# Kernel optimization log

Measured on AMD Instinct MI355X. Metric: run time of the kernel, lower is better.

The kernel has to match this reference:

```python
import jax, jax.numpy as jnp
import numpy as np

EPS_RMS = 1e-6
Q_CLIP_MIN = 1e-5

def setup_inputs() -> dict:
    key = jax.random.key(0)
    k1, k2 = jax.random.split(key)
    x = jax.random.normal(k1, (1, 2048, 4096), dtype=jnp.float32)
    # kaiming_uniform-ish init for weight [in_features, out_features]
    fan_in = 4096
    bound = 1.0 / np.sqrt(fan_in)
    weight = jax.random.uniform(k2, (4096, 4096), dtype=jnp.float32, minval=-bound, maxval=bound)
    rms_weight = jnp.ones((4096,), dtype=jnp.float32)
    return {"x": x, "weight": weight, "rms_weight": rms_weight}

def reference(x, weight, rms_weight):
    # RMSNorm over last dim
    xn = x * jax.lax.rsqrt(jnp.mean(x * x, axis=-1, keepdims=True) + EPS_RMS) * rms_weight
    K = weight.shape[0]
    orig_shape = xn.shape
    x2 = xn.reshape(-1, K)  # [M, K]

    # per-tensor absmax int8 activation quantization
    a_scale = 127.0 / jnp.clip(jnp.max(jnp.abs(x2)), Q_CLIP_MIN)
    A_q = jnp.clip(jnp.round(x2 * a_scale), -128.0, 127.0)

    # absmean ternary weight quantization
    b_scale = 1.0 / jnp.clip(jnp.mean(jnp.abs(weight)), Q_CLIP_MIN)
    B_t = jnp.clip(jnp.round(weight * b_scale), -1.0, 1.0)

    # integer matmul + dequant: (A_q @ B_t) / (a_scale * b_scale)
    out = (A_q @ B_t) / (a_scale * b_scale)  # [M, N]
    return out.reshape(*orig_shape[:-1], weight.shape[1])
```

## Files before the change

kernel.cpp:

```cpp
#include <hip/hip_runtime.h>
#include <cstdint>

#define M_DIM 2048
#define K_DIM 4096
#define N_DIM 4096

#define BM 256
#define BN 128
#define BK 128
#define KT (K_DIM / BK)
#define A_TILE_BYTES (BM * BK)
#define B_TILE_BYTES (BN * BK)
#define TILE_BYTES (A_TILE_BYTES + B_TILE_BYTES)
#define NBUF 3
#define LDS_BYTES (NBUF * TILE_BYTES)

typedef __attribute__((ext_vector_type(4))) int i32x4;

__device__ __forceinline__ void gload_lds16(const void* g, void* l) {
  __builtin_amdgcn_global_load_lds(
      (__attribute__((address_space(1))) void*)(g),
      (__attribute__((address_space(3))) void*)(l), 16, 0, 0);
}

__global__ void fused_reduce_kernel(const float* __restrict__ x,
                                    const float* __restrict__ rw,
                                    const float* __restrict__ w,
                                    float* __restrict__ invrms,
                                    float* __restrict__ rowmax,
                                    double* __restrict__ partials) {
  const int tid = threadIdx.x;
  __shared__ double red[4];
  __shared__ float redf[4];
  __shared__ float sInv;

  if (blockIdx.x < 2048) {
    const int row = blockIdx.x;
    const float4* xr = (const float4*)(x + (size_t)row * K_DIM);
    const float4* wr = (const float4*)rw;
    float4 xv[4];
    double ss = 0.0;
#pragma unroll
    for (int i = 0; i < 4; i++) {
      xv[i] = xr[i * 256 + tid];
      ss += (double)xv[i].x * xv[i].x + (double)xv[i].y * xv[i].y +
            (double)xv[i].z * xv[i].z + (double)xv[i].w * xv[i].w;
    }
    for (int off = 32; off; off >>= 1) ss += __shfl_down(ss, off);
    if ((tid & 63) == 0) red[tid >> 6] = ss;
    __syncthreads();
    if (tid == 0) {
      double t = red[0] + red[1] + red[2] + red[3];
      sInv = (float)(1.0 / sqrt(t * (1.0 / (double)K_DIM) + 1e-6));
    }
    __syncthreads();
    const float inv = sInv;
    if (tid == 0) invrms[row] = inv;

    float amax = 0.f;
#pragma unroll
    for (int i = 0; i < 4; i++) {
      float4 wv = wr[i * 256 + tid];
      amax = fmaxf(amax, fabsf((xv[i].x * inv) * wv.x));
      amax = fmaxf(amax, fabsf((xv[i].y * inv) * wv.y));
      amax = fmaxf(amax, fabsf((xv[i].z * inv) * wv.z));
      amax = fmaxf(amax, fabsf((xv[i].w * inv) * wv.w));
    }
    for (int off = 32; off; off >>= 1) amax = fmaxf(amax, __shfl_down(amax, off));
    if ((tid & 63) == 0) redf[tid >> 6] = amax;
    __syncthreads();
    if (tid == 0)
      rowmax[row] = fmaxf(fmaxf(redf[0], redf[1]), fmaxf(redf[2], redf[3]));
  } else {
    const int bid = blockIdx.x - 2048;
    const float4* w4 = (const float4*)w;
    const size_t base = (size_t)bid * 2048;
    double s = 0.0;
#pragma unroll
    for (int i = 0; i < 8; i++) {
      float4 v = w4[base + i * 256 + tid];
      s += (double)((fabsf(v.x) + fabsf(v.y)) + (fabsf(v.z) + fabsf(v.w)));
    }
    for (int off = 32; off; off >>= 1) s += __shfl_down(s, off);
    if ((tid & 63) == 0) red[tid >> 6] = s;
    __syncthreads();
    if (tid == 0) partials[bid] = red[0] + red[1] + red[2] + red[3];
  }
}

__global__ void scales_kernel(const float* __restrict__ rowmax,
                              const double* __restrict__ partials,
                              float* __restrict__ scales) {
  const int tid = threadIdx.x;
  float m = 0.f;
  double s = 0.0;
#pragma unroll
  for (int i = 0; i < 8; i++) {
    m = fmaxf(m, rowmax[i * 256 + tid]);
    s += partials[i * 256 + tid];
  }
  for (int off = 32; off; off >>= 1) {
    m = fmaxf(m, __shfl_down(m, off));
    s += __shfl_down(s, off);
  }
  __shared__ float redf[4];
  __shared__ double red[4];
  if ((tid & 63) == 0) { redf[tid >> 6] = m; red[tid >> 6] = s; }
  __syncthreads();
  if (tid == 0) {
    float amax = fmaxf(fmaxf(redf[0], redf[1]), fmaxf(redf[2], redf[3]));
    double wsum = red[0] + red[1] + red[2] + red[3];
    float as = 127.0f / fmaxf(amax, 1e-5f);
    float mean_f = (float)(wsum * (1.0 / 16777216.0));
    float bs = 1.0f / fmaxf(mean_f, 1e-5f);
    scales[0] = as;
    scales[1] = bs;
    scales[2] = 1.0f / (as * bs);
  }
}

__global__ void fused_quant_kernel(const float* __restrict__ x,
                                   const float* __restrict__ rw,
                                   const float* __restrict__ invrms,
                                   const float* __restrict__ scales,
                                   const float* __restrict__ w,
                                   char* __restrict__ Aq,
                                   char* __restrict__ Bt) {
  const int tid = threadIdx.x;
  if (blockIdx.x < 2048) {
    const int row = blockIdx.x;
    const float inv = invrms[row];
    const float as = scales[0];
    const float4* xr = (const float4*)(x + (size_t)row * K_DIM);
    const float4* wr = (const float4*)rw;
    union { char c[16]; int4 v; } o;
#pragma unroll
    for (int i = 0; i < 4; i++) {
      float4 xv = xr[tid * 4 + i];
      float4 wv = wr[tid * 4 + i];
      float t0 = (xv.x * inv) * wv.x;
      float t1 = (xv.y * inv) * wv.y;
      float t2 = (xv.z * inv) * wv.z;
      float t3 = (xv.w * inv) * wv.w;
      o.c[i * 4 + 0] = (char)(int)fminf(fmaxf(rintf(t0 * as), -128.f), 127.f);
      o.c[i * 4 + 1] = (char)(int)fminf(fmaxf(rintf(t1 * as), -128.f), 127.f);
      o.c[i * 4 + 2] = (char)(int)fminf(fmaxf(rintf(t2 * as), -128.f), 127.f);
      o.c[i * 4 + 3] = (char)(int)fminf(fmaxf(rintf(t3 * as), -128.f), 127.f);
    }
    *(int4*)(Aq + (size_t)row * K_DIM + tid * 16) = o.v;
  } else {
    __shared__ float lds[64][68];
    const int tile = blockIdx.x - 2048;
    const int n0 = (tile & 63) * 64;
    const int k0 = (tile >> 6) * 64;
    const float bs = scales[1];
#pragma unroll
    for (int i = 0; i < 4; i++) {
      const int id = i * 256 + tid;
      const int r = id >> 4;
      const int c4 = (id & 15) * 4;
      float4 v = *(const float4*)(w + (size_t)(k0 + r) * N_DIM + n0 + c4);
      lds[c4 + 0][r] = fminf(fmaxf(rintf(v.x * bs), -1.f), 1.f);
      lds[c4 + 1][r] = fminf(fmaxf(rintf(v.y * bs), -1.f), 1.f);
      lds[c4 + 2][r] = fminf(fmaxf(rintf(v.z * bs), -1.f), 1.f);
      lds[c4 + 3][r] = fminf(fmaxf(rintf(v.w * bs), -1.f), 1.f);
    }
    __syncthreads();
    const int rn = tid >> 2;
    const int kg = (tid & 3) * 16;
    union { char c[16]; int4 v; } o;
#pragma unroll
    for (int j = 0; j < 16; j++) o.c[j] = (char)(int)lds[rn][kg + j];
    *(int4*)(Bt + (size_t)(n0 + rn) * K_DIM + k0 + kg) = o.v;
  }
}

__global__ void __launch_bounds__(512, 2)
gemm_kernel(const char* __restrict__ Aq, const char* __restrict__ Bt,
            float* __restrict__ out, const float* __restrict__ scales) {
  extern __shared__ char lds[];
  const int tid = threadIdx.x;
  const int lane = tid & 63;
  const int wave = tid >> 6;
  const int wm = wave >> 1;
  const int wn = wave & 1;
  const int brow = blockIdx.y * BM;
  const int bcol = blockIdx.x * BN;

  i32x4 acc[4][4];
#pragma unroll
  for (int m = 0; m < 4; m++)
#pragma unroll
    for (int n = 0; n < 4; n++) acc[m][n] = {0, 0, 0, 0};

  const int sRow8 = lane >> 3;
  const int srcColB = ((lane & 7) ^ sRow8) * 16;

#define STAGE_A(kt, bi, s)                                                        \
  gload_lds16(Aq + (size_t)(brow + (s)*64 + wave * 8 + sRow8) * K_DIM +           \
                  (kt)*BK + srcColB,                                              \
              lds + (bi)*TILE_BYTES + (s)*8192 + wave * 1024 + lane * 16)
#define STAGE_B(kt, bi, s)                                                        \
  gload_lds16(Bt + (size_t)(bcol + (s)*64 + wave * 8 + sRow8) * K_DIM +           \
                  (kt)*BK + srcColB,                                              \
              lds + (bi)*TILE_BYTES + A_TILE_BYTES + (s)*8192 + wave * 1024 +     \
                  lane * 16)

  STAGE_A(0, 0, 0); STAGE_A(0, 0, 1); STAGE_A(0, 0, 2); STAGE_A(0, 0, 3);
  STAGE_B(0, 0, 0); STAGE_B(0, 0, 1);
  STAGE_A(1, 1, 0); STAGE_A(1, 1, 1); STAGE_A(1, 1, 2); STAGE_A(1, 1, 3);
  STAGE_B(1, 1, 0); STAGE_B(1, 1, 1);

  const int frow = lane & 15;
  int bi = 0;
  for (int t = 0; t < KT; ++t) {
    if (t < KT - 1) {
      asm volatile("s_waitcnt vmcnt(6)" ::: "memory");
    } else {
      asm volatile("s_waitcnt vmcnt(0)" ::: "memory");
    }
    __builtin_amdgcn_s_barrier();

    const int si = (bi + 2 >= NBUF) ? bi + 2 - NBUF : bi + 2;
    const bool doStage = (t + 2) < KT;
    const char* bufA = lds + bi * TILE_BYTES;
    const char* bufB = bufA + A_TILE_BYTES;

    if (doStage) {
      STAGE_A(t + 2, si, 0); STAGE_A(t + 2, si, 1); STAGE_A(t + 2, si, 2);
    }
    {
      const int sc = ((0 * 4 + (lane >> 4)) ^ (lane & 7)) * 16;
      i32x4 a[4], b[4];
#pragma unroll
      for (int m = 0; m < 4; m++)
        a[m] = *(const i32x4*)(bufA + (wm * 64 + m * 16 + frow) * BK + sc);
#pragma unroll
      for (int n = 0; n < 4; n++)
        b[n] = *(const i32x4*)(bufB + (wn * 64 + n * 16 + frow) * BK + sc);
      __builtin_amdgcn_s_setprio(1);
#pragma unroll
      for (int m = 0; m < 4; m++)
#pragma unroll
        for (int n = 0; n < 4; n++)
          acc[m][n] = __builtin_amdgcn_mfma_i32_16x16x64_i8(a[m], b[n], acc[m][n], 0, 0, 0);
      __builtin_amdgcn_s_setprio(0);
    }
    if (doStage) {
      STAGE_A(t + 2, si, 3); STAGE_B(t + 2, si, 0); STAGE_B(t + 2, si, 1);
    }
    {
      const int sc = ((1 * 4 + (lane >> 4)) ^ (lane & 7)) * 16;
      i32x4 a[4], b[4];
#pragma unroll
      for (int m = 0; m < 4; m++)
        a[m] = *(const i32x4*)(bufA + (wm * 64 + m * 16 + frow) * BK + sc);
#pragma unroll
      for (int n = 0; n < 4; n++)
        b[n] = *(const i32x4*)(bufB + (wn * 64 + n * 16 + frow) * BK + sc);
      __builtin_amdgcn_s_setprio(1);
#pragma unroll
      for (int m = 0; m < 4; m++)
#pragma unroll
        for (int n = 0; n < 4; n++)
          acc[m][n] = __builtin_amdgcn_mfma_i32_16x16x64_i8(a[m], b[n], acc[m][n], 0, 0, 0);
      __builtin_amdgcn_s_setprio(0);
    }
    bi = (bi + 1 >= NBUF) ? 0 : bi + 1;
  }
#undef STAGE_A
#undef STAGE_B

  const float dq = scales[2];
#pragma unroll
  for (int m = 0; m < 4; m++) {
#pragma unroll
    for (int n = 0; n < 4; n++) {
      const int row = wm * 64 + m * 16 + (lane >> 4) * 4;
      const int col = wn * 64 + n * 16 + (lane & 15);
#pragma unroll
      for (int j = 0; j < 4; j++) {
        out[(size_t)(brow + row + j) * N_DIM + bcol + col] = (float)acc[m][n][j] * dq;
      }
    }
  }
}

extern "C" void kernel_launch(void* const* d_in, const int* in_sizes, int n_in,
                              void* d_out, int out_size, void* d_ws, size_t ws_size,
                              hipStream_t stream) {
  const float* x      = (const float*)d_in[0];
  const float* weight = (const float*)d_in[1];
  const float* rms_w  = (const float*)d_in[2];
  float* out = (float*)d_out;

  uint8_t* ws = (uint8_t*)d_ws;
  float* scales   = (float*)(ws + 0);
  float* invrms   = (float*)(ws + 64);
  float* rowmax   = (float*)(ws + 64 + 8192);
  double* partials = (double*)(ws + 64 + 16384);
  char* Aq = (char*)(ws + 65536);
  char* Bt = (char*)(ws + 65536 + (size_t)M_DIM * K_DIM);

  (void)hipFuncSetAttribute((const void*)gemm_kernel,
                            hipFuncAttributeMaxDynamicSharedMemorySize, LDS_BYTES);

  fused_reduce_kernel<<<4096, 256, 0, stream>>>(x, rms_w, weight, invrms, rowmax, partials);
  scales_kernel<<<1, 256, 0, stream>>>(rowmax, partials, scales);
  fused_quant_kernel<<<6144, 256, 0, stream>>>(x, rms_w, invrms, scales, weight, Aq, Bt);
  gemm_kernel<<<dim3(N_DIM / BN, M_DIM / BM), 512, LDS_BYTES, stream>>>(Aq, Bt, out, scales);
}
```

Measured before the change: 74.34 us.

## Restructure GEMM K-loop into four-quadrant ping-pong schedule with interleaved staging

Reorganizes the int8 GEMM main loop so each wave loads A/B fragments for both K sub-steps per 64x64 quadrant, then runs MFMAs over four 32x32 quadrants while interleaving global-to-LDS staging between them. The intent is to overlap LDS reads and async global loads with MFMA execution, using explicit barriers, lgkmcnt waits and sched_barriers to pin the instruction order. It adds several workgroup barriers per iteration and holds more fragment registers at once, which could hurt occupancy or add sync stalls. The wait and barrier for the first tile is moved ahead of the loop, and the vmcnt wait now sits at the end of each iteration.

New measurement: 77.32 us. +4.0%, slower.

```diff
diff --git a/kernel.cpp b/kernel.cpp
--- a/kernel.cpp
+++ b/kernel.cpp
@@ -210,10 +210,98 @@
   STAGE_B(0, 0, 0); STAGE_B(0, 0, 1);
   STAGE_A(1, 1, 0); STAGE_A(1, 1, 1); STAGE_A(1, 1, 2); STAGE_A(1, 1, 3);
   STAGE_B(1, 1, 0); STAGE_B(1, 1, 1);
-
-  const int frow = lane & 15;
+  asm volatile("s_waitcnt vmcnt(6)" ::: "memory");
+  __builtin_amdgcn_s_barrier();
+
+  const int aBase = (wm * 64 + (lane & 15)) * BK;
+  const int bBase = (wn * 64 + (lane & 15)) * BK;
+  const int swz0 = ((0 * 4 + (lane >> 4)) ^ (lane & 7)) * 16;
+  const int swz1 = ((1 * 4 + (lane >> 4)) ^ (lane & 7)) * 16;
+
   int bi = 0;
   for (int t = 0; t < KT; ++t) {
+    const char* bufA = lds + bi * TILE_BYTES;
+    const char* bufB = bufA + A_TILE_BYTES;
+    const int si = (bi + 2 >= NBUF) ? bi + 2 - NBUF : bi + 2;
+    const bool doStage = (t + 2) < KT;
+
+    i32x4 a0_[4], a1_[4], b0_[4], b1_[4];
+
+#pragma unroll
+    for (int s = 0; s < 2; s++) {
+      a0_[s * 2 + 0] = *(const i32x4*)(bufA + aBase + s * 2048 + swz0);
+      a0_[s * 2 + 1] = *(const i32x4*)(bufA + aBase + s * 2048 + swz1);
+      b0_[s * 2 + 0] = *(const i32x4*)(bufB + bBase + s * 2048 + swz0);
+      b0_[s * 2 + 1] = *(const i32x4*)(bufB + bBase + s * 2048 + swz1);
+    }
+    if (doStage) { STAGE_A(t + 2, si, 0); STAGE_A(t + 2, si, 1); }
+    __builtin_amdgcn_s_barrier();
+    asm volatile("s_waitcnt lgkmcnt(0)" ::: "memory");
+    __builtin_amdgcn_sched_barrier(0);
+    __builtin_amdgcn_s_setprio(1);
+#pragma unroll
+    for (int mi = 0; mi < 2; mi++)
+#pragma unroll
+      for (int ni = 0; ni < 2; ni++)
+#pragma unroll
+        for (int ks = 0; ks < 2; ks++)
+          acc[mi][ni] = __builtin_amdgcn_mfma_i32_16x16x64_i8(
+              a0_[mi * 2 + ks], b0_[ni * 2 + ks], acc[mi][ni], 0, 0, 0);
+    __builtin_amdgcn_s_setprio(0);
+    __builtin_amdgcn_s_barrier();
+
+#pragma unroll
+    for (int s = 0; s < 2; s++) {
+      b1_[s * 2 + 0] = *(const i32x4*)(bufB + bBase + (s + 2) * 2048 + swz0);
+      b1_[s * 2 + 1] = *(const i32x4*)(bufB + bBase + (s + 2) * 2048 + swz1);
+    }
+    if (doStage) { STAGE_A(t + 2, si, 2); STAGE_A(t + 2, si, 3); }
+    __builtin_amdgcn_s_barrier();
+    asm volatile("s_waitcnt lgkmcnt(0)" ::: "memory");
+    __builtin_amdgcn_sched_barrier(0);
+    __builtin_amdgcn_s_setprio(1);
+#pragma unroll
+    for (int mi = 0; mi < 2; mi++)
+#pragma unroll
+      for (int ni = 0; ni < 2; ni++)
+#pragma unroll
+        for (int ks = 0; ks < 2; ks++)
+          acc[mi][ni + 2] = __builtin_amdgcn_mfma_i32_16x16x64_i8(
+              a0_[mi * 2 + ks], b1_[ni * 2 + ks], acc[mi][ni + 2], 0, 0, 0);
+    __builtin_amdgcn_s_setprio(0);
+    __builtin_amdgcn_s_barrier();
+
+#pragma unroll
+    for (int s = 0; s < 2; s++) {
+      a1_[s * 2 + 0] = *(const i32x4*)(bufA + aBase + (s + 2) * 2048 + swz0);
+      a1_[s * 2 + 1] = *(const i32x4*)(bufA + aBase + (s + 2) * 2048 + swz1);
+    }
+    if (doStage) { STAGE_B(t + 2, si, 0); STAGE_B(t + 2, si, 1); }
+    __builtin_amdgcn_s_barrier();
+    asm volatile("s_waitcnt lgkmcnt(0)" ::: "memory");
+    __builtin_amdgcn_sched_barrier(0);
+    __builtin_amdgcn_s_setprio(1);
+#pragma unroll
+    for (int mi = 0; mi < 2; mi++)
+#pragma unroll
+      for (int ni = 0; ni < 2; ni++)
+#pragma unroll
+        for (int ks = 0; ks < 2; ks++)
+          acc[mi + 2][ni] = __builtin_amdgcn_mfma_i32_16x16x64_i8(
+              a1_[mi * 2 + ks], b0_[ni * 2 + ks], acc[mi + 2][ni], 0, 0, 0);
+    __builtin_amdgcn_s_setprio(0);
+    __builtin_amdgcn_s_barrier();
+
+    __builtin_amdgcn_s_setprio(1);
+#pragma unroll
+    for (int mi = 0; mi < 2; mi++)
+#pragma unroll
+      for (int ni = 0; ni < 2; ni++)
+#pragma unroll
+        for (int ks = 0; ks < 2; ks++)
+          acc[mi + 2][ni + 2] = __builtin_amdgcn_mfma_i32_16x16x64_i8(
+              a1_[mi * 2 + ks], b1_[ni * 2 + ks], acc[mi + 2][ni + 2], 0, 0, 0);
+    __builtin_amdgcn_s_setprio(0);
     if (t < KT - 1) {
       asm volatile("s_waitcnt vmcnt(6)" ::: "memory");
     } else {
@@ -221,51 +309,6 @@
     }
     __builtin_amdgcn_s_barrier();
 
-    const int si = (bi + 2 >= NBUF) ? bi + 2 - NBUF : bi + 2;
-    const bool doStage = (t + 2) < KT;
-    const char* bufA = lds + bi * TILE_BYTES;
-    const char* bufB = bufA + A_TILE_BYTES;
-
-    if (doStage) {
-      STAGE_A(t + 2, si, 0); STAGE_A(t + 2, si, 1); STAGE_A(t + 2, si, 2);
-    }
-    {
-      const int sc = ((0 * 4 + (lane >> 4)) ^ (lane & 7)) * 16;
-      i32x4 a[4], b[4];
-#pragma unroll
-      for (int m = 0; m < 4; m++)
-        a[m] = *(const i32x4*)(bufA + (wm * 64 + m * 16 + frow) * BK + sc);
-#pragma unroll
-      for (int n = 0; n < 4; n++)
-        b[n] = *(const i32x4*)(bufB + (wn * 64 + n * 16 + frow) * BK + sc);
-      __builtin_amdgcn_s_setprio(1);
-#pragma unroll
-      for (int m = 0; m < 4; m++)
-#pragma unroll
-        for (int n = 0; n < 4; n++)
-          acc[m][n] = __builtin_amdgcn_mfma_i32_16x16x64_i8(a[m], b[n], acc[m][n], 0, 0, 0);
-      __builtin_amdgcn_s_setprio(0);
-    }
-    if (doStage) {
-      STAGE_A(t + 2, si, 3); STAGE_B(t + 2, si, 0); STAGE_B(t + 2, si, 1);
-    }
-    {
-      const int sc = ((1 * 4 + (lane >> 4)) ^ (lane & 7)) * 16;
-      i32x4 a[4], b[4];
-#pragma unroll
-      for (int m = 0; m < 4; m++)
-        a[m] = *(const i32x4*)(bufA + (wm * 64 + m * 16 + frow) * BK + sc);
-#pragma unroll
-      for (int n = 0; n < 4; n++)
-        b[n] = *(const i32x4*)(bufB + (wn * 64 + n * 16 + frow) * BK + sc);
-      __builtin_amdgcn_s_setprio(1);
-#pragma unroll
-      for (int m = 0; m < 4; m++)
-#pragma unroll
-        for (int n = 0; n < 4; n++)
-          acc[m][n] = __builtin_amdgcn_mfma_i32_16x16x64_i8(a[m], b[n], acc[m][n], 0, 0, 0);
-      __builtin_amdgcn_s_setprio(0);
-    }
     bi = (bi + 1 >= NBUF) ? 0 : bi + 1;
   }
 #undef STAGE_A
@@ -295,9 +338,9 @@
   float* out = (float*)d_out;
 
   uint8_t* ws = (uint8_t*)d_ws;
-  float* scales   = (float*)(ws + 0);
-  float* invrms   = (float*)(ws + 64);
-  float* rowmax   = (float*)(ws + 64 + 8192);
+  float* scales    = (float*)(ws + 0);
+  float* invrms    = (float*)(ws + 64);
+  float* rowmax    = (float*)(ws + 64 + 8192);
   double* partials = (double*)(ws + 64 + 16384);
   char* Aq = (char*)(ws + 65536);
   char* Bt = (char*)(ws + 65536 + (size_t)M_DIM * K_DIM);
```

## Use four-wave GEMM blocks with 128x64 warp tiles and fragment prefetch

Applied to the files above, without the earlier changes.

Restructures the int8 GEMM from 8 waves computing 64x64 each to 4 waves computing 128x64 each, and processes the full BK=128 slice per iteration with two k-substeps. The goal is to raise MFMA-to-LDS-read reuse per wave. The A/B fragments for the next tile are loaded into registers before the next iteration, and explicit lgkmcnt/vmcnt waits with sched_barriers overlap LDS reads with MFMA work. The cost is a much larger register footprint and fewer waves per CU to hide latency.

Result: slower. 77.04 us (+3.6%).

```diff
diff --git a/kernel.cpp b/kernel.cpp
--- a/kernel.cpp
+++ b/kernel.cpp
@@ -175,7 +175,7 @@
   }
 }
 
-__global__ void __launch_bounds__(512, 2)
+__global__ void __launch_bounds__(256, 1)
 gemm_kernel(const char* __restrict__ Aq, const char* __restrict__ Bt,
             float* __restrict__ out, const float* __restrict__ scales) {
   extern __shared__ char lds[];
@@ -187,9 +187,9 @@
   const int brow = blockIdx.y * BM;
   const int bcol = blockIdx.x * BN;
 
-  i32x4 acc[4][4];
-#pragma unroll
-  for (int m = 0; m < 4; m++)
+  i32x4 acc[8][4];
+#pragma unroll
+  for (int m = 0; m < 8; m++)
 #pragma unroll
     for (int n = 0; n < 4; n++) acc[m][n] = {0, 0, 0, 0};
 
@@ -197,74 +197,113 @@
   const int srcColB = ((lane & 7) ^ sRow8) * 16;
 
 #define STAGE_A(kt, bi, s)                                                        \
-  gload_lds16(Aq + (size_t)(brow + (s)*64 + wave * 8 + sRow8) * K_DIM +           \
+  gload_lds16(Aq + (size_t)(brow + (s)*32 + wave * 8 + sRow8) * K_DIM +           \
                   (kt)*BK + srcColB,                                              \
-              lds + (bi)*TILE_BYTES + (s)*8192 + wave * 1024 + lane * 16)
+              lds + (bi)*TILE_BYTES + (s)*4096 + wave * 1024 + lane * 16)
 #define STAGE_B(kt, bi, s)                                                        \
-  gload_lds16(Bt + (size_t)(bcol + (s)*64 + wave * 8 + sRow8) * K_DIM +           \
+  gload_lds16(Bt + (size_t)(bcol + (s)*32 + wave * 8 + sRow8) * K_DIM +           \
                   (kt)*BK + srcColB,                                              \
-              lds + (bi)*TILE_BYTES + A_TILE_BYTES + (s)*8192 + wave * 1024 +     \
+              lds + (bi)*TILE_BYTES + A_TILE_BYTES + (s)*4096 + wave * 1024 +     \
                   lane * 16)
 
-  STAGE_A(0, 0, 0); STAGE_A(0, 0, 1); STAGE_A(0, 0, 2); STAGE_A(0, 0, 3);
-  STAGE_B(0, 0, 0); STAGE_B(0, 0, 1);
-  STAGE_A(1, 1, 0); STAGE_A(1, 1, 1); STAGE_A(1, 1, 2); STAGE_A(1, 1, 3);
-  STAGE_B(1, 1, 0); STAGE_B(1, 1, 1);
-
-  const int frow = lane & 15;
+#pragma unroll
+  for (int s = 0; s < 8; s++) STAGE_A(0, 0, s);
+#pragma unroll
+  for (int s = 0; s < 4; s++) STAGE_B(0, 0, s);
+#pragma unroll
+  for (int s = 0; s < 8; s++) STAGE_A(1, 1, s);
+#pragma unroll
+  for (int s = 0; s < 4; s++) STAGE_B(1, 1, s);
+  asm volatile("s_waitcnt vmcnt(12)" ::: "memory");
+  __builtin_amdgcn_s_barrier();
+
+  const int aBase = (wm * 128 + (lane & 15)) * BK;
+  const int bBase = (wn * 64 + (lane & 15)) * BK;
+  const int swz0 = ((0 + (lane >> 4)) ^ (lane & 7)) * 16;
+  const int swz1 = ((4 + (lane >> 4)) ^ (lane & 7)) * 16;
+
+  i32x4 a0[8], a1[8], bb[8];
+
+#pragma unroll
+  for (int m = 0; m < 4; m++) {
+    a0[m * 2 + 0] = *(const i32x4*)(lds + aBase + m * 2048 + swz0);
+    a0[m * 2 + 1] = *(const i32x4*)(lds + aBase + m * 2048 + swz1);
+  }
+#pragma unroll
+  for (int n = 0; n < 4; n++) {
+    bb[n * 2 + 0] = *(const i32x4*)(lds + A_TILE_BYTES + bBase + n * 2048 + swz0);
+    bb[n * 2 + 1] = *(const i32x4*)(lds + A_TILE_BYTES + bBase + n * 2048 + swz1);
+  }
+
   int bi = 0;
   for (int t = 0; t < KT; ++t) {
-    if (t < KT - 1) {
-      asm volatile("s_waitcnt vmcnt(6)" ::: "memory");
-    } else {
-      asm volatile("s_waitcnt vmcnt(0)" ::: "memory");
-    }
-    __builtin_amdgcn_s_barrier();
-
+    const char* bufA = lds + bi * TILE_BYTES;
     const int si = (bi + 2 >= NBUF) ? bi + 2 - NBUF : bi + 2;
     const bool doStage = (t + 2) < KT;
-    const char* bufA = lds + bi * TILE_BYTES;
-    const char* bufB = bufA + A_TILE_BYTES;
+
+    __builtin_amdgcn_s_barrier();
+    __builtin_amdgcn_sched_barrier(0);
 
     if (doStage) {
       STAGE_A(t + 2, si, 0); STAGE_A(t + 2, si, 1); STAGE_A(t + 2, si, 2);
-    }
-    {
-      const int sc = ((0 * 4 + (lane >> 4)) ^ (lane & 7)) * 16;
-      i32x4 a[4], b[4];
-#pragma unroll
-      for (int m = 0; m < 4; m++)
-        a[m] = *(const i32x4*)(bufA + (wm * 64 + m * 16 + frow) * BK + sc);
+      STAGE_A(t + 2, si, 3); STAGE_A(t + 2, si, 4); STAGE_A(t + 2, si, 5);
+    }
+#pragma unroll
+    for (int m = 0; m < 4; m++) {
+      a1[m * 2 + 0] = *(const i32x4*)(bufA + aBase + (m + 4) * 2048 + swz0);
+      a1[m * 2 + 1] = *(const i32x4*)(bufA + aBase + (m + 4) * 2048 + swz1);
+    }
+    asm volatile("s_waitcnt lgkmcnt(8)" ::: "memory");
+    __builtin_amdgcn_sched_barrier(0);
+    __builtin_amdgcn_s_setprio(1);
+#pragma unroll
+    for (int m = 0; m < 4; m++)
 #pragma unroll
       for (int n = 0; n < 4; n++)
-        b[n] = *(const i32x4*)(bufB + (wn * 64 + n * 16 + frow) * BK + sc);
-      __builtin_amdgcn_s_setprio(1);
-#pragma unroll
-      for (int m = 0; m < 4; m++)
-#pragma unroll
-        for (int n = 0; n < 4; n++)
-          acc[m][n] = __builtin_amdgcn_mfma_i32_16x16x64_i8(a[m], b[n], acc[m][n], 0, 0, 0);
-      __builtin_amdgcn_s_setprio(0);
-    }
+#pragma unroll
+        for (int ks = 0; ks < 2; ks++)
+          acc[m][n] = __builtin_amdgcn_mfma_i32_16x16x64_i8(
+              a0[m * 2 + ks], bb[n * 2 + ks], acc[m][n], 0, 0, 0);
+    __builtin_amdgcn_s_setprio(0);
+
     if (doStage) {
-      STAGE_A(t + 2, si, 3); STAGE_B(t + 2, si, 0); STAGE_B(t + 2, si, 1);
-    }
-    {
-      const int sc = ((1 * 4 + (lane >> 4)) ^ (lane & 7)) * 16;
-      i32x4 a[4], b[4];
-#pragma unroll
-      for (int m = 0; m < 4; m++)
-        a[m] = *(const i32x4*)(bufA + (wm * 64 + m * 16 + frow) * BK + sc);
+      STAGE_A(t + 2, si, 6); STAGE_A(t + 2, si, 7);
+      STAGE_B(t + 2, si, 0); STAGE_B(t + 2, si, 1);
+      STAGE_B(t + 2, si, 2); STAGE_B(t + 2, si, 3);
+    }
+    asm volatile("s_waitcnt lgkmcnt(0)" ::: "memory");
+    __builtin_amdgcn_sched_barrier(0);
+    __builtin_amdgcn_s_setprio(1);
+#pragma unroll
+    for (int m = 0; m < 4; m++)
 #pragma unroll
       for (int n = 0; n < 4; n++)
-        b[n] = *(const i32x4*)(bufB + (wn * 64 + n * 16 + frow) * BK + sc);
-      __builtin_amdgcn_s_setprio(1);
-#pragma unroll
-      for (int m = 0; m < 4; m++)
-#pragma unroll
-        for (int n = 0; n < 4; n++)
-          acc[m][n] = __builtin_amdgcn_mfma_i32_16x16x64_i8(a[m], b[n], acc[m][n], 0, 0, 0);
-      __builtin_amdgcn_s_setprio(0);
+#pragma unroll
+        for (int ks = 0; ks < 2; ks++)
+          acc[m + 4][n] = __builtin_amdgcn_mfma_i32_16x16x64_i8(
+              a1[m * 2 + ks], bb[n * 2 + ks], acc[m + 4][n], 0, 0, 0);
+    __builtin_amdgcn_s_setprio(0);
+
+    if (t + 1 < KT) {
+      if (doStage) {
+        asm volatile("s_waitcnt vmcnt(12)" ::: "memory");
+      } else {
+        asm volatile("s_waitcnt vmcnt(0)" ::: "memory");
+      }
+      __builtin_amdgcn_sched_barrier(0);
+      const int ni = (bi + 1 >= NBUF) ? 0 : bi + 1;
+      const char* nA = lds + ni * TILE_BYTES;
+      const char* nB = nA + A_TILE_BYTES;
+#pragma unroll
+      for (int m = 0; m < 4; m++) {
+        a0[m * 2 + 0] = *(const i32x4*)(nA + aBase + m * 2048 + swz0);
+        a0[m * 2 + 1] = *(const i32x4*)(nA + aBase + m * 2048 + swz1);
+      }
+#pragma unroll
+      for (int n = 0; n < 4; n++) {
+        bb[n * 2 + 0] = *(const i32x4*)(nB + bBase + n * 2048 + swz0);
+        bb[n * 2 + 1] = *(const i32x4*)(nB + bBase + n * 2048 + swz1);
+      }
     }
     bi = (bi + 1 >= NBUF) ? 0 : bi + 1;
   }
@@ -273,10 +312,10 @@
 
   const float dq = scales[2];
 #pragma unroll
-  for (int m = 0; m < 4; m++) {
+  for (int m = 0; m < 8; m++) {
 #pragma unroll
     for (int n = 0; n < 4; n++) {
-      const int row = wm * 64 + m * 16 + (lane >> 4) * 4;
+      const int row = wm * 128 + m * 16 + (lane >> 4) * 4;
       const int col = wn * 64 + n * 16 + (lane & 15);
 #pragma unroll
       for (int j = 0; j < 4; j++) {
@@ -295,9 +334,9 @@
   float* out = (float*)d_out;
 
   uint8_t* ws = (uint8_t*)d_ws;
-  float* scales   = (float*)(ws + 0);
-  float* invrms   = (float*)(ws + 64);
-  float* rowmax   = (float*)(ws + 64 + 8192);
+  float* scales    = (float*)(ws + 0);
+  float* invrms    = (float*)(ws + 64);
+  float* rowmax    = (float*)(ws + 64 + 8192);
   double* partials = (double*)(ws + 64 + 16384);
   char* Aq = (char*)(ws + 65536);
   char* Bt = (char*)(ws + 65536 + (size_t)M_DIM * K_DIM);
@@ -308,5 +347,5 @@
   fused_reduce_kernel<<<4096, 256, 0, stream>>>(x, rms_w, weight, invrms, rowmax, partials);
   scales_kernel<<<1, 256, 0, stream>>>(rowmax, partials, scales);
   fused_quant_kernel<<<6144, 256, 0, stream>>>(x, rms_w, invrms, scales, weight, Aq, Bt);
-  gemm_kernel<<<dim3(N_DIM / BN, M_DIM / BM), 512, LDS_BYTES, stream>>>(Aq, Bt, out, scales);
-}
+  gemm_kernel<<<dim3(N_DIM / BN, M_DIM / BM), 256, LDS_BYTES, stream>>>(Aq, Bt, out, scales);
+}
```
